# Kernel tuning notes

Hardware: AMD Instinct MI355X
Metric: run time of the kernel (lower is better)

## Reference

```python
import jax, jax.numpy as jnp
import numpy as np

N = 50000
E = 640000
D_IN = 128
D_HID = 128
D_S = 64


def setup_inputs() -> dict:
    key = jax.random.key(0)
    ks = jax.random.split(key, 8)
    x = jax.random.normal(ks[0], (N, D_IN), dtype=jnp.float32)
    edge_index = jax.random.randint(ks[1], (2, E), 0, N, dtype=jnp.int64)
    # SAGEConv params: lin_l (applied to aggregated neighbors, has bias), lin_r (root)
    def glorot(k, fan_in, fan_out):
        lim = (6.0 / (fan_in + fan_out)) ** 0.5
        return jax.random.uniform(k, (fan_in, fan_out), jnp.float32, -lim, lim)
    return {
        "x": x,
        "edge_index": edge_index,
        "W_l1": glorot(ks[2], D_IN, D_HID),
        "b_l1": jnp.zeros((D_HID,), jnp.float32),
        "W_r1": glorot(ks[3], D_IN, D_HID),
        "W_l2": glorot(ks[4], D_HID, D_HID),
        "b_l2": jnp.zeros((D_HID,), jnp.float32),
        "W_r2": glorot(ks[5], D_HID, D_HID),
        "W_s": glorot(ks[6], D_HID, D_S),
    }


def _sage_conv(x, src, dst, W_l, b_l, W_r):
    # mean aggregation of source-node features into target nodes
    agg = jax.ops.segment_sum(x[src], dst, num_segments=N)  # [N, d]
    cnt = jax.ops.segment_sum(jnp.ones((src.shape[0],), x.dtype), dst, num_segments=N)
    mean = agg / jnp.maximum(cnt, 1.0)[:, None]
    return mean @ W_l + b_l + x @ W_r


def reference(x, edge_index, W_l1, b_l1, W_r1, W_l2, b_l2, W_r2, W_s):
    src, dst = edge_index[0], edge_index[1]
    h = _sage_conv(x, src, dst, W_l1, b_l1, W_r1)
    h = jax.nn.relu(h)
    h = _sage_conv(h, src, dst, W_l2, b_l2, W_r2)
    out_s = h @ W_s
    return (out_s, h)
```

## Files before the change

kernel.cpp:

```cpp
#include <hip/hip_runtime.h>

#define N_NODES 50000
#define E_EDGES 640000
#define D 128
#define DS 64
#define NTILES 3125
#define BUCKET 64

typedef __bf16 bf16x8 __attribute__((ext_vector_type(8)));
typedef float f32x4 __attribute__((ext_vector_type(4)));

static __device__ __forceinline__ ushort f2bf(float f) {
    uint u = __float_as_uint(f);
    uint r = u + 0x7fffu + ((u >> 16) & 1u);
    return (ushort)(r >> 16);
}


__global__ void prep_kernel(const float* __restrict__ x,
                            const float* __restrict__ Wl1, const float* __restrict__ Wr1,
                            const float* __restrict__ Wl2, const float* __restrict__ Wr2,
                            const float* __restrict__ Ws,
                            int* __restrict__ cursor, ushort* __restrict__ xb,
                            ushort* __restrict__ WT1f, ushort* __restrict__ WT2f,
                            ushort* __restrict__ WsTf) {
    int tid = blockIdx.x * blockDim.x + threadIdx.x;
    if (tid < N_NODES) cursor[tid] = 0;
    if (tid < 32768) {
        int n = tid >> 8, k = tid & 255;
        float v = (k < 128) ? Wl1[k * 128 + n] : Wr1[(k - 128) * 128 + n];
        int F = (n >> 4) * 8 + (k >> 5);
        int l = (n & 15) | (((k >> 3) & 3) << 4);
        WT1f[(F * 64 + l) * 8 + (k & 7)] = f2bf(v);
    } else if (tid < 65536) {
        int j = tid - 32768;
        int n = j >> 8, k = j & 255;
        float v = (k < 128) ? Wl2[k * 128 + n] : Wr2[(k - 128) * 128 + n];
        int F = (n >> 4) * 8 + (k >> 5);
        int l = (n & 15) | (((k >> 3) & 3) << 4);
        WT2f[(F * 64 + l) * 8 + (k & 7)] = f2bf(v);
    } else if (tid < 73728) {
        int j = tid - 65536;
        int m = j >> 7, k = j & 127;
        int F = (m >> 4) * 4 + (k >> 5);
        int l = (m & 15) | (((k >> 3) & 3) << 4);
        WsTf[(F * 64 + l) * 8 + (k & 7)] = f2bf(Ws[k * 64 + m]);
    }
    const int n4 = N_NODES * D / 4;
    int stride = gridDim.x * blockDim.x;
    for (int i = tid; i < n4; i += stride) {
        float4 v = ((const float4*)x)[i];
        ushort4 o;
        o.x = f2bf(v.x); o.y = f2bf(v.y); o.z = f2bf(v.z); o.w = f2bf(v.w);
        ((ushort4*)xb)[i] = o;
    }
}


__global__ void fill_kernel(const int* __restrict__ src, const int* __restrict__ dst,
                            int* __restrict__ cursor, ushort* __restrict__ esrc, int e) {
    int i = blockIdx.x * blockDim.x + threadIdx.x;
    if (i < e) {
        int d = dst[i];
        int pos = atomicAdd(&cursor[d], 1);
        if (pos < BUCKET) esrc[d * BUCKET + pos] = (ushort)src[i];
    }
}


__global__ void aggregate_mean_bf16(const ushort* __restrict__ feat, const int* __restrict__ cursor,
                                    const ushort* __restrict__ esrc, ushort* __restrict__ mean, int n) {
    int wid = threadIdx.x >> 6;
    int lane = threadIdx.x & 63;
    int d = blockIdx.x * 4 + wid;
    if (d >= n) return;
    int cnt = cursor[d]; if (cnt > BUCKET) cnt = BUCKET;
    int beg = d * BUCKET;
    int g = lane >> 4;
    int gl = lane & 15;

    float acc[8] = {0.f, 0.f, 0.f, 0.f, 0.f, 0.f, 0.f, 0.f};
    for (int i = 0; i < cnt; i += 16) {
        uint4 v[4];
#pragma unroll
        for (int j = 0; j < 4; ++j) {
            int idx = i + g + j * 4;
            v[j] = make_uint4(0u, 0u, 0u, 0u);
            if (idx < cnt) {
                int e = esrc[beg + idx];
                v[j] = ((const uint4*)(feat + (size_t)e * D))[gl];
            }
        }
#pragma unroll
        for (int j = 0; j < 4; ++j) {
            acc[0] += __uint_as_float(v[j].x << 16);
            acc[1] += __uint_as_float(v[j].x & 0xffff0000u);
            acc[2] += __uint_as_float(v[j].y << 16);
            acc[3] += __uint_as_float(v[j].y & 0xffff0000u);
            acc[4] += __uint_as_float(v[j].z << 16);
            acc[5] += __uint_as_float(v[j].z & 0xffff0000u);
            acc[6] += __uint_as_float(v[j].w << 16);
            acc[7] += __uint_as_float(v[j].w & 0xffff0000u);
        }
    }
#pragma unroll
    for (int m = 16; m <= 32; m <<= 1) {
#pragma unroll
        for (int j = 0; j < 8; ++j) acc[j] += __shfl_xor(acc[j], m);
    }
    if (g == 0) {
        float inv = (cnt > 0) ? 1.0f / (float)cnt : 0.0f;
        uint4 o;
        o.x = (uint)f2bf(acc[0] * inv) | ((uint)f2bf(acc[1] * inv) << 16);
        o.y = (uint)f2bf(acc[2] * inv) | ((uint)f2bf(acc[3] * inv) << 16);
        o.z = (uint)f2bf(acc[4] * inv) | ((uint)f2bf(acc[5] * inv) << 16);
        o.w = (uint)f2bf(acc[6] * inv) | ((uint)f2bf(acc[7] * inv) << 16);
        ((uint4*)(mean + (size_t)d * D))[gl] = o;
    }
}


template <bool RELU, bool WF32, bool WBF16, bool OUTS>
__global__ __launch_bounds__(512) void sage_mfma(
    const ushort* __restrict__ A1, const ushort* __restrict__ A2,
    const ushort* __restrict__ WTf, const float* __restrict__ bias,
    float* __restrict__ Hf, ushort* __restrict__ Hb,
    const ushort* __restrict__ WsTf, float* __restrict__ OutS)
{
    __shared__ __attribute__((aligned(16))) char smem[OUTS ? 81920 : 65536];
    int w = threadIdx.x >> 6, lane = threadIdx.x & 63;

#pragma unroll
    for (int it = 0; it < 8; ++it) {
        int off = w * 8192 + it * 1024;
        __builtin_amdgcn_global_load_lds(
            (const __attribute__((address_space(1))) void*)((const char*)WTf + off + lane * 16),
            (__attribute__((address_space(3))) void*)(smem + off), 16, 0, 0);
    }
    if (OUTS) {
#pragma unroll
        for (int it = 0; it < 2; ++it) {
            int off = w * 2048 + it * 1024;
            __builtin_amdgcn_global_load_lds(
                (const __attribute__((address_space(1))) void*)((const char*)WsTf + off + lane * 16),
                (__attribute__((address_space(3))) void*)(smem + 65536 + off), 16, 0, 0);
        }
    }

    int rl = lane & 15;
    int kg = lane >> 4;
    int tile = blockIdx.x * 8 + w;

    bf16x8 a[8];
    if (tile < NTILES) {
        const ushort* r1 = A1 + (size_t)(tile * 16 + rl) * 128 + kg * 8;
        const ushort* r2 = A2 + (size_t)(tile * 16 + rl) * 128 + kg * 8;
#pragma unroll
        for (int s = 0; s < 4; ++s) a[s] = *reinterpret_cast<const bf16x8*>(r1 + s * 32);
#pragma unroll
        for (int s = 0; s < 4; ++s) a[4 + s] = *reinterpret_cast<const bf16x8*>(r2 + s * 32);
    }
    __syncthreads();
    if (tile >= NTILES) return;

    f32x4 acc[8];
#pragma unroll
    for (int f = 0; f < 8; ++f)
        acc[f] = *reinterpret_cast<const f32x4*>(bias + f * 16 + kg * 4);

#pragma unroll
    for (int s = 0; s < 8; ++s) {
#pragma unroll
        for (int f = 0; f < 8; ++f) {
            bf16x8 b = *reinterpret_cast<const bf16x8*>(smem + ((f * 8 + s) * 64 + lane) * 16);
            acc[f] = __builtin_amdgcn_mfma_f32_16x16x32_bf16(b, a[s], acc[f], 0, 0, 0);
        }
    }

    int node = tile * 16 + rl;
#pragma unroll
    for (int f = 0; f < 8; ++f) {
        f32x4 v = acc[f];
        if (RELU) {
            v[0] = fmaxf(v[0], 0.f); v[1] = fmaxf(v[1], 0.f);
            v[2] = fmaxf(v[2], 0.f); v[3] = fmaxf(v[3], 0.f);
        }
        acc[f] = v;
        size_t o = (size_t)node * 128 + f * 16 + kg * 4;
        if (WF32)
            *reinterpret_cast<f32x4*>(Hf + o) = v;
        if (WBF16) {
            ushort4 ob;
            ob.x = f2bf(v[0]); ob.y = f2bf(v[1]); ob.z = f2bf(v[2]); ob.w = f2bf(v[3]);
            *reinterpret_cast<ushort4*>(Hb + o) = ob;
        }
    }

    if (OUTS) {
        uint abx[8], aby[8];
#pragma unroll
        for (int f = 0; f < 8; ++f) {
            abx[f] = (uint)f2bf(acc[f][0]) | ((uint)f2bf(acc[f][1]) << 16);
            aby[f] = (uint)f2bf(acc[f][2]) | ((uint)f2bf(acc[f][3]) << 16);
        }
        int sbase = rl + ((lane & 16) << 1);
        bool top = lane >= 32;
        f32x4 accO[4];
#pragma unroll
        for (int fo = 0; fo < 4; ++fo) accO[fo] = (f32x4){0.f, 0.f, 0.f, 0.f};

#pragma unroll
        for (int s = 0; s < 4; ++s) {
            uint lx = abx[s * 2], ly = aby[s * 2];
            uint hx = abx[s * 2 + 1], hy = aby[s * 2 + 1];
            uint l0 = (uint)__shfl((int)lx, sbase);
            uint h0 = (uint)__shfl((int)hx, sbase);
            uint l1 = (uint)__shfl((int)ly, sbase);
            uint h1 = (uint)__shfl((int)hy, sbase);
            uint l2 = (uint)__shfl((int)lx, sbase + 16);
            uint h2_ = (uint)__shfl((int)hx, sbase + 16);
            uint l3 = (uint)__shfl((int)ly, sbase + 16);
            uint h3 = (uint)__shfl((int)hy, sbase + 16);
            uint q0 = top ? h0 : l0;
            uint q1 = top ? h1 : l1;
            uint q2 = top ? h2_ : l2;
            uint q3 = top ? h3 : l3;
            union { uint4 u; bf16x8 b; } cvt;
            cvt.u = make_uint4(q0, q1, q2, q3);
#pragma unroll
            for (int fo = 0; fo < 4; ++fo) {
                bf16x8 wsA = *reinterpret_cast<const bf16x8*>(
                    smem + 65536 + ((fo * 4 + s) * 64 + lane) * 16);
                accO[fo] = __builtin_amdgcn_mfma_f32_16x16x32_bf16(wsA, cvt.b, accO[fo], 0, 0, 0);
            }
        }
#pragma unroll
        for (int fo = 0; fo < 4; ++fo)
            *reinterpret_cast<f32x4*>(OutS + (size_t)node * DS + fo * 16 + kg * 4) = accO[fo];
    }
}

extern "C" void kernel_launch(void* const* d_in, const int* in_sizes, int n_in,
                              void* d_out, int out_size, void* d_ws, size_t ws_size,
                              hipStream_t stream) {
    const float* x   = (const float*)d_in[0];
    const int*   ei  = (const int*)d_in[1];
    const float* Wl1 = (const float*)d_in[2];
    const float* bl1 = (const float*)d_in[3];
    const float* Wr1 = (const float*)d_in[4];
    const float* Wl2 = (const float*)d_in[5];
    const float* bl2 = (const float*)d_in[6];
    const float* Wr2 = (const float*)d_in[7];
    const float* Ws  = (const float*)d_in[8];

    const int* src = ei;
    const int* dst = ei + E_EDGES;

    char* wsb = (char*)d_ws;
    size_t off = 0;
    auto alloc = [&](size_t bytes) -> void* {
        void* p = wsb + off;
        off = (off + bytes + 255) & ~(size_t)255;
        return p;
    };
    int*    cursor = (int*)alloc(4 * (size_t)N_NODES);
    ushort* esrc   = (ushort*)alloc(2 * (size_t)N_NODES * BUCKET);
    ushort* xb     = (ushort*)alloc(2 * (size_t)N_NODES * D);
    ushort* meanb  = (ushort*)alloc(2 * (size_t)N_NODES * D);
    ushort* h1b    = (ushort*)alloc(2 * (size_t)N_NODES * D);
    ushort* WT1f   = (ushort*)alloc(2 * 128 * 256);
    ushort* WT2f   = (ushort*)alloc(2 * 128 * 256);
    ushort* WsTf   = (ushort*)alloc(2 * 64 * 128);

    float* out_s = (float*)d_out;
    float* h2    = (float*)d_out + (size_t)N_NODES * DS;

    prep_kernel<<<2048, 256, 0, stream>>>(x, Wl1, Wr1, Wl2, Wr2, Ws,
                                          cursor, xb, WT1f, WT2f, WsTf);

    fill_kernel<<<(E_EDGES + 255) / 256, 256, 0, stream>>>(src, dst, cursor, esrc, E_EDGES);

    const int GB = (NTILES + 7) / 8;

    aggregate_mean_bf16<<<(N_NODES + 3) / 4, 256, 0, stream>>>(xb, cursor, esrc, meanb, N_NODES);
    sage_mfma<true, false, true, false><<<GB, 512, 0, stream>>>(
        meanb, xb, WT1f, bl1, nullptr, h1b, nullptr, nullptr);

    aggregate_mean_bf16<<<(N_NODES + 3) / 4, 256, 0, stream>>>(h1b, cursor, esrc, meanb, N_NODES);
    sage_mfma<false, true, false, true><<<GB, 512, 0, stream>>>(
        meanb, h1b, WT2f, bl2, h2, nullptr, WsTf, out_s);
}
```

Before: 129.1 us.

## Fuse neighbor mean aggregation into the MFMA SAGE layer kernel

Removes the separate aggregation kernel and its bf16 mean buffer. Each lane now gathers its own destination node's neighbor rows directly into MFMA A-fragment registers, two edges per iteration, before the GEMM. This saves a global write/read round trip of the mean matrix and two launches. The cost is a lane-per-node gather: each lane walks a serial edge loop, so wave divergence across the 16 nodes of a tile and lower memory-level parallelism may hurt the gather phase.

```diff
diff --git a/kernel.cpp b/kernel.cpp
--- a/kernel.cpp
+++ b/kernel.cpp
@@ -68,61 +68,10 @@
 }
 
 
-__global__ void aggregate_mean_bf16(const ushort* __restrict__ feat, const int* __restrict__ cursor,
-                                    const ushort* __restrict__ esrc, ushort* __restrict__ mean, int n) {
-    int wid = threadIdx.x >> 6;
-    int lane = threadIdx.x & 63;
-    int d = blockIdx.x * 4 + wid;
-    if (d >= n) return;
-    int cnt = cursor[d]; if (cnt > BUCKET) cnt = BUCKET;
-    int beg = d * BUCKET;
-    int g = lane >> 4;
-    int gl = lane & 15;
-
-    float acc[8] = {0.f, 0.f, 0.f, 0.f, 0.f, 0.f, 0.f, 0.f};
-    for (int i = 0; i < cnt; i += 16) {
-        uint4 v[4];
-#pragma unroll
-        for (int j = 0; j < 4; ++j) {
-            int idx = i + g + j * 4;
-            v[j] = make_uint4(0u, 0u, 0u, 0u);
-            if (idx < cnt) {
-                int e = esrc[beg + idx];
-                v[j] = ((const uint4*)(feat + (size_t)e * D))[gl];
-            }
-        }
-#pragma unroll
-        for (int j = 0; j < 4; ++j) {
-            acc[0] += __uint_as_float(v[j].x << 16);
-            acc[1] += __uint_as_float(v[j].x & 0xffff0000u);
-            acc[2] += __uint_as_float(v[j].y << 16);
-            acc[3] += __uint_as_float(v[j].y & 0xffff0000u);
-            acc[4] += __uint_as_float(v[j].z << 16);
-            acc[5] += __uint_as_float(v[j].z & 0xffff0000u);
-            acc[6] += __uint_as_float(v[j].w << 16);
-            acc[7] += __uint_as_float(v[j].w & 0xffff0000u);
-        }
-    }
-#pragma unroll
-    for (int m = 16; m <= 32; m <<= 1) {
-#pragma unroll
-        for (int j = 0; j < 8; ++j) acc[j] += __shfl_xor(acc[j], m);
-    }
-    if (g == 0) {
-        float inv = (cnt > 0) ? 1.0f / (float)cnt : 0.0f;
-        uint4 o;
-        o.x = (uint)f2bf(acc[0] * inv) | ((uint)f2bf(acc[1] * inv) << 16);
-        o.y = (uint)f2bf(acc[2] * inv) | ((uint)f2bf(acc[3] * inv) << 16);
-        o.z = (uint)f2bf(acc[4] * inv) | ((uint)f2bf(acc[5] * inv) << 16);
-        o.w = (uint)f2bf(acc[6] * inv) | ((uint)f2bf(acc[7] * inv) << 16);
-        ((uint4*)(mean + (size_t)d * D))[gl] = o;
-    }
-}
-
-
 template <bool RELU, bool WF32, bool WBF16, bool OUTS>
-__global__ __launch_bounds__(512) void sage_mfma(
-    const ushort* __restrict__ A1, const ushort* __restrict__ A2,
+__global__ __launch_bounds__(512) void sage_fused(
+    const ushort* __restrict__ feat,
+    const int* __restrict__ cursor, const ushort* __restrict__ esrc,
     const ushort* __restrict__ WTf, const float* __restrict__ bias,
     float* __restrict__ Hf, ushort* __restrict__ Hb,
     const ushort* __restrict__ WsTf, float* __restrict__ OutS)
@@ -150,18 +99,58 @@
     int rl = lane & 15;
     int kg = lane >> 4;
     int tile = blockIdx.x * 8 + w;
-
+    bool valid = tile < NTILES;
+    int node = tile * 16 + rl;
+
+    float accm[4][8];
+#pragma unroll
+    for (int s = 0; s < 4; ++s)
+#pragma unroll
+        for (int j = 0; j < 8; ++j) accm[s][j] = 0.f;
+
+    int cnt = 0;
     bf16x8 a[8];
-    if (tile < NTILES) {
-        const ushort* r1 = A1 + (size_t)(tile * 16 + rl) * 128 + kg * 8;
-        const ushort* r2 = A2 + (size_t)(tile * 16 + rl) * 128 + kg * 8;
-#pragma unroll
-        for (int s = 0; s < 4; ++s) a[s] = *reinterpret_cast<const bf16x8*>(r1 + s * 32);
+    if (valid) {
+        cnt = cursor[node]; if (cnt > BUCKET) cnt = BUCKET;
+        int beg = node * BUCKET;
+        for (int idx = 0; idx < cnt; idx += 2) {
+            int e0 = esrc[beg + idx];
+            bool have1 = (idx + 1) < cnt;
+            int e1 = have1 ? esrc[beg + idx + 1] : e0;
+            const uint4* r0 = (const uint4*)(feat + (size_t)e0 * D);
+            const uint4* r1 = (const uint4*)(feat + (size_t)e1 * D);
+            uint4 v0[4], v1[4];
+#pragma unroll
+            for (int s = 0; s < 4; ++s) v0[s] = r0[s * 4 + kg];
+#pragma unroll
+            for (int s = 0; s < 4; ++s)
+                v1[s] = have1 ? r1[s * 4 + kg] : make_uint4(0u, 0u, 0u, 0u);
+#pragma unroll
+            for (int s = 0; s < 4; ++s) {
+                accm[s][0] += __uint_as_float(v0[s].x << 16) + __uint_as_float(v1[s].x << 16);
+                accm[s][1] += __uint_as_float(v0[s].x & 0xffff0000u) + __uint_as_float(v1[s].x & 0xffff0000u);
+                accm[s][2] += __uint_as_float(v0[s].y << 16) + __uint_as_float(v1[s].y << 16);
+                accm[s][3] += __uint_as_float(v0[s].y & 0xffff0000u) + __uint_as_float(v1[s].y & 0xffff0000u);
+                accm[s][4] += __uint_as_float(v0[s].z << 16) + __uint_as_float(v1[s].z << 16);
+                accm[s][5] += __uint_as_float(v0[s].z & 0xffff0000u) + __uint_as_float(v1[s].z & 0xffff0000u);
+                accm[s][6] += __uint_as_float(v0[s].w << 16) + __uint_as_float(v1[s].w << 16);
+                accm[s][7] += __uint_as_float(v0[s].w & 0xffff0000u) + __uint_as_float(v1[s].w & 0xffff0000u);
+            }
+        }
+        float inv = (cnt > 0) ? 1.0f / (float)cnt : 0.0f;
+#pragma unroll
+        for (int s = 0; s < 4; ++s) {
+            union { ushort u[8]; bf16x8 b; } p;
+#pragma unroll
+            for (int j = 0; j < 8; ++j) p.u[j] = f2bf(accm[s][j] * inv);
+            a[s] = p.b;
+        }
+        const ushort* r2 = feat + (size_t)node * 128 + kg * 8;
 #pragma unroll
         for (int s = 0; s < 4; ++s) a[4 + s] = *reinterpret_cast<const bf16x8*>(r2 + s * 32);
     }
     __syncthreads();
-    if (tile >= NTILES) return;
+    if (!valid) return;
 
     f32x4 acc[8];
 #pragma unroll
@@ -177,7 +166,6 @@
         }
     }
 
-    int node = tile * 16 + rl;
 #pragma unroll
     for (int f = 0; f < 8; ++f) {
         f32x4 v = acc[f];
@@ -266,7 +254,6 @@
     int*    cursor = (int*)alloc(4 * (size_t)N_NODES);
     ushort* esrc   = (ushort*)alloc(2 * (size_t)N_NODES * BUCKET);
     ushort* xb     = (ushort*)alloc(2 * (size_t)N_NODES * D);
-    ushort* meanb  = (ushort*)alloc(2 * (size_t)N_NODES * D);
     ushort* h1b    = (ushort*)alloc(2 * (size_t)N_NODES * D);
     ushort* WT1f   = (ushort*)alloc(2 * 128 * 256);
     ushort* WT2f   = (ushort*)alloc(2 * 128 * 256);
@@ -282,11 +269,9 @@
 
     const int GB = (NTILES + 7) / 8;
 
-    aggregate_mean_bf16<<<(N_NODES + 3) / 4, 256, 0, stream>>>(xb, cursor, esrc, meanb, N_NODES);
-    sage_mfma<true, false, true, false><<<GB, 512, 0, stream>>>(
-        meanb, xb, WT1f, bl1, nullptr, h1b, nullptr, nullptr);
-
-    aggregate_mean_bf16<<<(N_NODES + 3) / 4, 256, 0, stream>>>(h1b, cursor, esrc, meanb, N_NODES);
-    sage_mfma<false, true, false, true><<<GB, 512, 0, stream>>>(
-        meanb, h1b, WT2f, bl2, h2, nullptr, WsTf, out_s);
-}
+    sage_fused<true, false, true, false><<<GB, 512, 0, stream>>>(
+        xb, cursor, esrc, WT1f, bl1, nullptr, h1b, nullptr, nullptr);
+
+    sage_fused<false, true, false, true><<<GB, 512, 0, stream>>>(
+        h1b, cursor, esrc, WT2f, bl2, h2, nullptr, WsTf, out_s);
+}
```

New measurement: 142.6 us. 1.1x slower.
